# Kernel optimization log

Measured on AMD Instinct MI355X. Metric: run time of the kernel, lower is better.

The kernel has to match this reference:

```python
import jax, jax.numpy as jnp
import numpy as np

B, D, U = 64, 512, 512  # batch, input, units
EPS = 1e-5

def _ln(x, g, b, axes):
    m = jnp.mean(x, axis=axes, keepdims=True)
    v = jnp.mean((x - m) ** 2, axis=axes, keepdims=True)
    return (x - m) * jax.lax.rsqrt(v + EPS) * g + b

def setup_inputs() -> dict:
    key = jax.random.key(0)
    ks = jax.random.split(key, 8)
    w = lambda k, shape: 0.02 * jax.random.normal(k, shape, dtype=jnp.float32)
    return {
        "x": jax.random.normal(ks[0], (B, D), dtype=jnp.float32),
        "w1": w(ks[1], (1, D, U, 2)),
        "b1": jnp.zeros((1, D, U, 2), jnp.float32),
        "w21": w(ks[2], (1, D, U, 2)),
        "w22": w(ks[3], (1, D, U, 2)),
        "b21": jnp.zeros((1, D, U, 1), jnp.float32),
        "b22": jnp.zeros((1, D, U, 1), jnp.float32),
        "w3": w(ks[4], (1, D, U, 2)),
        "b3": jnp.zeros((1, D, U, 1), jnp.float32),
        "bias": jnp.zeros((U,), jnp.float32),
        "g0": jnp.ones((D,), jnp.float32), "be0": jnp.zeros((D,), jnp.float32),
        "g1": jnp.ones((D, U, 2), jnp.float32), "be1": jnp.zeros((D, U, 2), jnp.float32),
        "g2": jnp.ones((D, U, 2), jnp.float32), "be2": jnp.zeros((D, U, 2), jnp.float32),
        "g3": jnp.ones((D, U, 1), jnp.float32), "be3": jnp.zeros((D, U, 1), jnp.float32),
    }

def reference(x, w1, b1, w21, w22, b21, b22, w3, b3, bias,
              g0, be0, g1, be1, g2, be2, g3, be3):
    lrelu = lambda t: jnp.where(t >= 0, t, 0.01 * t)  # nn.LeakyReLU default slope
    xn = _ln(x, g0, be0, (-1,))[:, :, None, None]           # [B,D,1,1]
    l1 = lrelu(_ln(xn * w1 + b1, g1, be1, (1, 2, 3)))        # [B,D,U,2]
    l21 = jnp.sum(l1 * w21, axis=-1, keepdims=True) + b21    # [B,D,U,1]
    l22 = jnp.sum(l1 * w22, axis=-1, keepdims=True) + b22    # [B,D,U,1]
    l2 = lrelu(_ln(jnp.concatenate((l21, l22), axis=-1), g2, be2, (1, 2, 3)))  # [B,D,U,2]
    l3 = jnp.sum(l2 * w3, axis=-1, keepdims=True) + b3       # [B,D,U,1]
    out = _ln(l3, g3, be3, (1, 2, 3)) + xn                   # [B,D,U,1]
    out = lrelu(jnp.sum(out, axis=1) + bias[:, None])        # [B,U,1]
    return jnp.squeeze(out, axis=-1)                         # [B,U]
```

## Files before the change

kernel.cpp:

```cpp
#include <hip/hip_runtime.h>

#define EPS 1e-5f
constexpr float INV_N1 = 1.f / 524288.f;
constexpr float INV_N3 = 1.f / 262144.f;

__device__ __forceinline__ float lrelu(float y) { return fmaxf(y, 0.01f * y); }

template <int CTRL>
__device__ __forceinline__ float dppMov(float v) {
    return __int_as_float(__builtin_amdgcn_update_dpp(
        0, __float_as_int(v), CTRL, 0xF, 0xF, true));
}
__device__ __forceinline__ float rowSumDpp(float v) {
    v += dppMov<0x111>(v);
    v += dppMov<0x112>(v);
    v += dppMov<0x114>(v);
    v += dppMov<0x118>(v);
    return v;
}
__device__ __forceinline__ float quadSum(float v) {
    v += dppMov<0xB1>(v);
    v += dppMov<0x4E>(v);
    return v;
}
__device__ __forceinline__ float waveAllSum(float v) {
    v += __shfl_xor(v, 32); v += __shfl_xor(v, 16); v += __shfl_xor(v, 8);
    v += __shfl_xor(v, 4);  v += __shfl_xor(v, 2);  v += __shfl_xor(v, 1);
    return v;
}

__global__ void __launch_bounds__(256) kW(
    const float* __restrict__ w1, const float* __restrict__ b1,
    const float* __restrict__ g3, const float* __restrict__ be3,
    float* __restrict__ S1, float* __restrict__ S2, float* __restrict__ S11,
    float* __restrict__ S0b, float* __restrict__ Sb2,
    float* __restrict__ Gp, float* __restrict__ Bp) {
    int bid = blockIdx.x, tid = threadIdx.x;
    if (bid < 512) {
        const float4* wr = (const float4*)(w1 + bid * 1024);
        const float4* br = (const float4*)(b1 + bid * 1024);
        float4 w = wr[tid], b = br[tid];
        float s1  = w.x + w.y + w.z + w.w;
        float s2  = w.x * w.x + w.y * w.y + w.z * w.z + w.w * w.w;
        float s11 = w.x * b.x + w.y * b.y + w.z * b.z + w.w * b.w;
        float s0  = b.x + b.y + b.z + b.w;
        float sb2 = b.x * b.x + b.y * b.y + b.z * b.z + b.w * b.w;
        __shared__ float red[4][5];
        s1 = waveAllSum(s1); s2 = waveAllSum(s2); s11 = waveAllSum(s11);
        s0 = waveAllSum(s0); sb2 = waveAllSum(sb2);
        int wave = tid >> 6, lane = tid & 63;
        if (lane == 0) {
            red[wave][0] = s1; red[wave][1] = s2; red[wave][2] = s11;
            red[wave][3] = s0; red[wave][4] = sb2;
        }
        __syncthreads();
        if (tid == 0) {
            float a0 = 0, a1 = 0, a2 = 0, a3 = 0, a4 = 0;
            for (int w4 = 0; w4 < 4; ++w4) {
                a0 += red[w4][0]; a1 += red[w4][1]; a2 += red[w4][2];
                a3 += red[w4][3]; a4 += red[w4][4];
            }
            S1[bid] = a0; S2[bid] = a1; S11[bid] = a2;
            S0b[bid] = a3; Sb2[bid] = a4;
        }
    } else {
        int jj = bid - 512;
        float ag0 = 0, ag1 = 0, ab0 = 0, ab1 = 0;
#pragma unroll
        for (int r = 0; r < 8; ++r) {
            const float* gr = g3 + (jj * 8 + r) * 512;
            const float* br = be3 + (jj * 8 + r) * 512;
            ag0 += gr[tid];  ag1 += gr[tid + 256];
            ab0 += br[tid];  ab1 += br[tid + 256];
        }
        Gp[jj * 512 + tid] = ag0; Gp[jj * 512 + tid + 256] = ag1;
        Bp[jj * 512 + tid] = ab0; Bp[jj * 512 + tid + 256] = ab1;
    }
}

__global__ void __launch_bounds__(256) kB(
    const float* __restrict__ x, const float* __restrict__ g0,
    const float* __restrict__ be0,
    const float* __restrict__ S1, const float* __restrict__ S2,
    const float* __restrict__ S11, const float* __restrict__ S0b,
    const float* __restrict__ Sb2,
    const float* __restrict__ Gp, const float* __restrict__ Bp,
    float* __restrict__ xnp, float* __restrict__ rs1a, float* __restrict__ mm1a,
    float* __restrict__ Xs, float* __restrict__ G3s, float* __restrict__ Be3s) {
    int bid = blockIdx.x, tid = threadIdx.x;
    if (bid < 64) {
        int b = bid;
        float2 xv = ((const float2*)(x + b * 512))[tid];
        float sx = xv.x + xv.y;
        float sxx = xv.x * xv.x + xv.y * xv.y;
        __shared__ float red[4][3];
        __shared__ float bc[2];
        sx = waveAllSum(sx); sxx = waveAllSum(sxx);
        int wave = tid >> 6, lane = tid & 63;
        if (lane == 0) { red[wave][0] = sx; red[wave][1] = sxx; }
        __syncthreads();
        if (tid == 0) {
            float a = red[0][0] + red[1][0] + red[2][0] + red[3][0];
            float c = red[0][1] + red[1][1] + red[2][1] + red[3][1];
            float m = a * (1.f / 512.f);
            float var = c * (1.f / 512.f) - m * m;
            bc[0] = m; bc[1] = rsqrtf(var + EPS);
        }
        __syncthreads();
        float m = bc[0], rsd = bc[1];
        float2 g = ((const float2*)g0)[tid];
        float2 be = ((const float2*)be0)[tid];
        float xn0 = (xv.x - m) * rsd * g.x + be.x;
        float xn1 = (xv.y - m) * rsd * g.y + be.y;
        ((float2*)(xnp + b * 512))[tid] = make_float2(xn0, xn1);
        float2 s1 = ((const float2*)S1)[tid], s0b = ((const float2*)S0b)[tid];
        float2 s2 = ((const float2*)S2)[tid], s11 = ((const float2*)S11)[tid];
        float2 sb2 = ((const float2*)Sb2)[tid];
        float pm = fmaf(xn0, s1.x, s0b.x) + fmaf(xn1, s1.y, s0b.y);
        float pe = xn0 * xn0 * s2.x + 2.f * xn0 * s11.x + sb2.x
                 + xn1 * xn1 * s2.y + 2.f * xn1 * s11.y + sb2.y;
        float sxn = xn0 + xn1;
        pm = waveAllSum(pm); pe = waveAllSum(pe); sxn = waveAllSum(sxn);
        __syncthreads();
        if (lane == 0) { red[wave][0] = pm; red[wave][1] = pe; red[wave][2] = sxn; }
        __syncthreads();
        if (tid == 0) {
            float a = red[0][0] + red[1][0] + red[2][0] + red[3][0];
            float c = red[0][1] + red[1][1] + red[2][1] + red[3][1];
            float s = red[0][2] + red[1][2] + red[2][2] + red[3][2];
            float m1 = a * INV_N1;
            float e1 = c * INV_N1;
            float r = rsqrtf(e1 - m1 * m1 + EPS);
            rs1a[b] = r; mm1a[b] = m1 * r; Xs[b] = s;
        }
    } else if (bid == 64) {
        for (int u = tid; u < 512; u += 256) {
            float s = 0;
#pragma unroll 8
            for (int jj = 0; jj < 64; ++jj) s += Gp[jj * 512 + u];
            G3s[u] = s;
        }
    } else {
        for (int u = tid; u < 512; u += 256) {
            float s = 0;
#pragma unroll 8
            for (int jj = 0; jj < 64; ++jj) s += Bp[jj * 512 + u];
            Be3s[u] = s;
        }
    }
}

__global__ void __launch_bounds__(256) k1(
    const float* __restrict__ w1, const float* __restrict__ b1,
    const float* __restrict__ g1, const float* __restrict__ be1,
    const float* __restrict__ w21, const float* __restrict__ w22,
    const float* __restrict__ b21, const float* __restrict__ b22,
    const float* __restrict__ xnp, const float* __restrict__ rs1a,
    const float* __restrict__ mm1a, float* __restrict__ part1) {
    int bid = blockIdx.x, tid = threadIdx.x;
    int d = bid;
    __shared__ float xcol[64], scA[64], scB[64];
    __shared__ float2 red2[64][4][4];
    if (tid < 64) {
        xcol[tid] = xnp[tid * 512 + d];
        scA[tid] = rs1a[tid];
        scB[tid] = mm1a[tid];
    }
    int i0 = d * 512 + tid, i1 = i0 + 256;
    float2 W1a = ((const float2*)w1)[i0], B1a = ((const float2*)b1)[i0];
    float2 G1a = ((const float2*)g1)[i0], E1a = ((const float2*)be1)[i0];
    float2 Aa  = ((const float2*)w21)[i0], Ca = ((const float2*)w22)[i0];
    float Baa = b21[i0], Bca = b22[i0];
    float2 W1b = ((const float2*)w1)[i1], B1b = ((const float2*)b1)[i1];
    float2 G1b = ((const float2*)g1)[i1], E1b = ((const float2*)be1)[i1];
    float2 Ab  = ((const float2*)w21)[i1], Cb = ((const float2*)w22)[i1];
    float Bab = b21[i1], Bcb = b22[i1];
    __syncthreads();
    int wave = tid >> 6, lane = tid & 63;
    for (int b = 0; b < 64; ++b) {
        float xd = xcol[b], r1 = scA[b], mmv = scB[b];
        float t0 = fmaf(xd, W1a.x, B1a.x), t1 = fmaf(xd, W1a.y, B1a.y);
        float z0 = fmaf(t0, r1, -mmv), z1 = fmaf(t1, r1, -mmv);
        float y0 = fmaf(z0, G1a.x, E1a.x), y1 = fmaf(z1, G1a.y, E1a.y);
        float l0 = lrelu(y0), l1 = lrelu(y1);
        float c0 = fmaf(l0, Aa.x, fmaf(l1, Aa.y, Baa));
        float c1 = fmaf(l0, Ca.x, fmaf(l1, Ca.y, Bca));
        float v1 = c0 + c1;
        float v2 = fmaf(c0, c0, c1 * c1);
        t0 = fmaf(xd, W1b.x, B1b.x); t1 = fmaf(xd, W1b.y, B1b.y);
        z0 = fmaf(t0, r1, -mmv); z1 = fmaf(t1, r1, -mmv);
        y0 = fmaf(z0, G1b.x, E1b.x); y1 = fmaf(z1, G1b.y, E1b.y);
        l0 = lrelu(y0); l1 = lrelu(y1);
        c0 = fmaf(l0, Ab.x, fmaf(l1, Ab.y, Bab));
        c1 = fmaf(l0, Cb.x, fmaf(l1, Cb.y, Bcb));
        v1 += c0 + c1;
        v2 = fmaf(c0, c0, fmaf(c1, c1, v2));
        v1 = rowSumDpp(v1);
        v2 = rowSumDpp(v2);
        if ((lane & 15) == 15)
            red2[b][wave][lane >> 4] = make_float2(v1, v2);
    }
    __syncthreads();
    if (tid < 128) {
        int b = tid >> 1, k = tid & 1;
        float s = 0;
#pragma unroll
        for (int w = 0; w < 4; ++w)
#pragma unroll
            for (int r = 0; r < 4; ++r)
                s += ((const float*)&red2[b][w][r])[k];
        part1[bid * 128 + tid] = s;
    }
}

struct Wt { float2 W1, B1, G1, E1, A, C, G2, E2, W3; float Ba, Bc, B3, G3v; };

__global__ void __launch_bounds__(256) k2(
    const float* __restrict__ w1, const float* __restrict__ b1,
    const float* __restrict__ g1, const float* __restrict__ be1,
    const float* __restrict__ w21, const float* __restrict__ w22,
    const float* __restrict__ b21, const float* __restrict__ b22,
    const float* __restrict__ g2, const float* __restrict__ be2,
    const float* __restrict__ w3, const float* __restrict__ b3,
    const float* __restrict__ g3,
    const float* __restrict__ xnp, const float* __restrict__ rs1a,
    const float* __restrict__ mm1a, const float* __restrict__ part1,
    float* __restrict__ pp, float* __restrict__ qp) {
    int bu = blockIdx.x & 31, bd = blockIdx.x >> 5, tid = threadIdx.x;
    int lane = tid & 63, wave = tid >> 6;
    int ul = (lane >> 2) & 15, d0 = lane & 3;
    int u = bu * 16 + ul;
    int dl0 = wave * 8 + d0 * 2;
    __shared__ float4 sc[64];
    __shared__ float sxn[64][32];
    __shared__ float comb[4][64][16][3];
    __shared__ float tmp2[2][128];
    {
        int s = tid & 127, half = tid >> 7;
        float acc = 0;
        const float* p = part1 + half * 256 * 128 + s;
#pragma unroll 8
        for (int blk = 0; blk < 256; ++blk) acc += p[blk * 128];
        tmp2[half][s] = acc;
    }
    {
        float* cz = &comb[0][0][0][0];
        for (int t = tid; t < 4 * 64 * 16 * 3; t += 256) cz[t] = 0.f;
    }
    for (int idx = tid; idx < 2048; idx += 256)
        sxn[idx >> 5][idx & 31] = xnp[(idx >> 5) * 512 + bd * 32 + (idx & 31)];
    Wt wt[2];
#pragma unroll
    for (int j = 0; j < 2; ++j) {
        int d = bd * 32 + dl0 + j;
        int i = d * 512 + u;
        wt[j].W1 = ((const float2*)w1)[i];  wt[j].B1 = ((const float2*)b1)[i];
        wt[j].G1 = ((const float2*)g1)[i];  wt[j].E1 = ((const float2*)be1)[i];
        wt[j].A  = ((const float2*)w21)[i]; wt[j].C  = ((const float2*)w22)[i];
        wt[j].G2 = ((const float2*)g2)[i];  wt[j].E2 = ((const float2*)be2)[i];
        wt[j].W3 = ((const float2*)w3)[i];
        wt[j].Ba = b21[i]; wt[j].Bc = b22[i]; wt[j].B3 = b3[i]; wt[j].G3v = g3[i];
    }
    __syncthreads();
    if (tid < 64) {
        float ssum = tmp2[0][2 * tid] + tmp2[1][2 * tid];
        float s2sum = tmp2[0][2 * tid + 1] + tmp2[1][2 * tid + 1];
        float mm = ssum * INV_N1;
        float var = s2sum * INV_N1 - mm * mm;
        float r2 = rsqrtf(var + EPS);
        sc[tid] = make_float4(rs1a[tid], mm1a[tid], r2, mm * r2);
    }
    __syncthreads();
    for (int b = 0; b < 64; ++b) {
        float4 s4 = sc[b];
        float p = 0, q = 0, q2 = 0;
#pragma unroll
        for (int j = 0; j < 2; ++j) {
            float xd = sxn[b][dl0 + j];
            float t0 = fmaf(xd, wt[j].W1.x, wt[j].B1.x), t1 = fmaf(xd, wt[j].W1.y, wt[j].B1.y);
            float z0 = fmaf(t0, s4.x, -s4.y), z1 = fmaf(t1, s4.x, -s4.y);
            float y0 = fmaf(z0, wt[j].G1.x, wt[j].E1.x), y1 = fmaf(z1, wt[j].G1.y, wt[j].E1.y);
            float l0 = lrelu(y0), l1 = lrelu(y1);
            float c0 = fmaf(l0, wt[j].A.x, fmaf(l1, wt[j].A.y, wt[j].Ba));
            float c1 = fmaf(l0, wt[j].C.x, fmaf(l1, wt[j].C.y, wt[j].Bc));
            float z20 = fmaf(c0, s4.z, -s4.w), z21 = fmaf(c1, s4.z, -s4.w);
            float y20 = fmaf(z20, wt[j].G2.x, wt[j].E2.x), y21 = fmaf(z21, wt[j].G2.y, wt[j].E2.y);
            float m0 = lrelu(y20), m1v = lrelu(y21);
            float l3 = fmaf(m0, wt[j].W3.x, fmaf(m1v, wt[j].W3.y, wt[j].B3));
            p = fmaf(l3, wt[j].G3v, p); q += l3; q2 = fmaf(l3, l3, q2);
        }
        p = quadSum(p); q = quadSum(q); q2 = quadSum(q2);
        if (d0 < 3) {
            float v = (d0 == 0) ? p : ((d0 == 1) ? q : q2);
            comb[wave][b][ul][d0] += v;
        }
    }
    __syncthreads();
#pragma unroll
    for (int r = 0; r < 4; ++r) {
        int idx = r * 256 + tid;
        int b = idx >> 4, uu = idx & 15;
        float s = comb[0][b][uu][0] + comb[1][b][uu][0]
                + comb[2][b][uu][0] + comb[3][b][uu][0];
        pp[(bd * 64 + b) * 512 + bu * 16 + uu] = s;
    }
    if (tid < 128) {
        int b = tid >> 1, st = 1 + (tid & 1);
        float s = 0;
#pragma unroll
        for (int w = 0; w < 4; ++w)
#pragma unroll
            for (int uu = 0; uu < 16; ++uu) s += comb[w][b][uu][st];
        qp[(bd * 32 + bu) * 128 + b * 2 + (st - 1)] = s;
    }
}

__global__ void __launch_bounds__(512) k3(
    const float* __restrict__ pp, const float* __restrict__ qp,
    const float* __restrict__ G3s, const float* __restrict__ Be3s,
    const float* __restrict__ Xs, const float* __restrict__ bias,
    float* __restrict__ out) {
    int b = blockIdx.x, u = threadIdx.x;
    float q  = qp[u * 128 + b * 2 + 0];
    float q2 = qp[u * 128 + b * 2 + 1];
    __shared__ float red[8][2];
    __shared__ float bc2[2];
    float sq = waveAllSum(q), sq2 = waveAllSum(q2);
    int wave = u >> 6, lane = u & 63;
    if (lane == 0) { red[wave][0] = sq; red[wave][1] = sq2; }
    __syncthreads();
    if (u == 0) {
        float a = 0, c = 0;
        for (int w = 0; w < 8; ++w) { a += red[w][0]; c += red[w][1]; }
        float m3 = a * INV_N3;
        float e3 = c * INV_N3;
        bc2[0] = m3; bc2[1] = rsqrtf(e3 - m3 * m3 + EPS);
    }
    __syncthreads();
    float p = 0;
#pragma unroll 4
    for (int bd = 0; bd < 16; ++bd) p += pp[(bd * 64 + b) * 512 + u];
    float m3 = bc2[0], rs3 = bc2[1];
    float val = rs3 * (p - m3 * G3s[u]) + Be3s[u] + Xs[b] + bias[u];
    out[b * 512 + u] = lrelu(val);
}

extern "C" void kernel_launch(void* const* d_in, const int* in_sizes, int n_in,
                              void* d_out, int out_size, void* d_ws, size_t ws_size,
                              hipStream_t stream) {
    const float* x   = (const float*)d_in[0];
    const float* w1  = (const float*)d_in[1];
    const float* b1  = (const float*)d_in[2];
    const float* w21 = (const float*)d_in[3];
    const float* w22 = (const float*)d_in[4];
    const float* b21 = (const float*)d_in[5];
    const float* b22 = (const float*)d_in[6];
    const float* w3  = (const float*)d_in[7];
    const float* b3  = (const float*)d_in[8];
    const float* bias= (const float*)d_in[9];
    const float* g0  = (const float*)d_in[10];
    const float* be0 = (const float*)d_in[11];
    const float* g1  = (const float*)d_in[12];
    const float* be1 = (const float*)d_in[13];
    const float* g2  = (const float*)d_in[14];
    const float* be2 = (const float*)d_in[15];
    const float* g3  = (const float*)d_in[16];
    const float* be3 = (const float*)d_in[17];
    float* out = (float*)d_out;
    char* ws = (char*)d_ws;

    float* xn    = (float*)(ws);
    float* S1    = (float*)(ws + 131072);
    float* S2    = (float*)(ws + 133120);
    float* S11   = (float*)(ws + 135168);
    float* S0b   = (float*)(ws + 137216);
    float* Sb2   = (float*)(ws + 139264);
    float* rs1a  = (float*)(ws + 141312);
    float* mm1a  = (float*)(ws + 141568);
    float* Xs    = (float*)(ws + 141824);
    float* G3s   = (float*)(ws + 142080);
    float* Be3s  = (float*)(ws + 144128);
    float* Gp    = (float*)(ws + 146176);
    float* Bp    = (float*)(ws + 277248);
    float* part1 = (float*)(ws + 408320);
    float* qp    = (float*)(ws + 670464);
    float* pp    = (float*)(ws + 932608);

    hipLaunchKernelGGL(kW, dim3(576), dim3(256), 0, stream,
                       w1, b1, g3, be3, S1, S2, S11, S0b, Sb2, Gp, Bp);
    hipLaunchKernelGGL(kB, dim3(66), dim3(256), 0, stream,
                       x, g0, be0, S1, S2, S11, S0b, Sb2, Gp, Bp,
                       xn, rs1a, mm1a, Xs, G3s, Be3s);
    hipLaunchKernelGGL(k1, dim3(512), dim3(256), 0, stream,
                       w1, b1, g1, be1, w21, w22, b21, b22, xn, rs1a, mm1a, part1);
    hipLaunchKernelGGL(k2, dim3(512), dim3(256), 0, stream,
                       w1, b1, g1, be1, w21, w22, b21, b22, g2, be2, w3, b3, g3,
                       xn, rs1a, mm1a, part1, pp, qp);
    hipLaunchKernelGGL(k3, dim3(64), dim3(512), 0, stream,
                       pp, qp, G3s, Be3s, Xs, bias, out);
}
```

Baseline: 72.10 us.

## Eliminate the stats kernel by fusing its work into neighbouring kernels

Result: slower. 90.37 us (+25.3%).

```diff
diff --git a/kernel.cpp b/kernel.cpp
--- a/kernel.cpp
+++ b/kernel.cpp
@@ -29,13 +29,19 @@
     return v;
 }
 
-__global__ void __launch_bounds__(256) kW(
+__global__ void __launch_bounds__(256) kA(
     const float* __restrict__ w1, const float* __restrict__ b1,
     const float* __restrict__ g3, const float* __restrict__ be3,
+    const float* __restrict__ x, const float* __restrict__ g0,
+    const float* __restrict__ be0,
     float* __restrict__ S1, float* __restrict__ S2, float* __restrict__ S11,
     float* __restrict__ S0b, float* __restrict__ Sb2,
-    float* __restrict__ Gp, float* __restrict__ Bp) {
+    float* __restrict__ Gp, float* __restrict__ Bp,
+    float* __restrict__ xnp, float* __restrict__ Xs) {
     int bid = blockIdx.x, tid = threadIdx.x;
+    int wave = tid >> 6, lane = tid & 63;
+    __shared__ float red[4][5];
+    __shared__ float bc[2];
     if (bid < 512) {
         const float4* wr = (const float4*)(w1 + bid * 1024);
         const float4* br = (const float4*)(b1 + bid * 1024);
@@ -45,10 +51,8 @@
         float s11 = w.x * b.x + w.y * b.y + w.z * b.z + w.w * b.w;
         float s0  = b.x + b.y + b.z + b.w;
         float sb2 = b.x * b.x + b.y * b.y + b.z * b.z + b.w * b.w;
-        __shared__ float red[4][5];
         s1 = waveAllSum(s1); s2 = waveAllSum(s2); s11 = waveAllSum(s11);
         s0 = waveAllSum(s0); sb2 = waveAllSum(sb2);
-        int wave = tid >> 6, lane = tid & 63;
         if (lane == 0) {
             red[wave][0] = s1; red[wave][1] = s2; red[wave][2] = s11;
             red[wave][3] = s0; red[wave][4] = sb2;
@@ -63,7 +67,7 @@
             S1[bid] = a0; S2[bid] = a1; S11[bid] = a2;
             S0b[bid] = a3; Sb2[bid] = a4;
         }
-    } else {
+    } else if (bid < 576) {
         int jj = bid - 512;
         float ag0 = 0, ag1 = 0, ab0 = 0, ab1 = 0;
 #pragma unroll
@@ -75,78 +79,31 @@
         }
         Gp[jj * 512 + tid] = ag0; Gp[jj * 512 + tid + 256] = ag1;
         Bp[jj * 512 + tid] = ab0; Bp[jj * 512 + tid + 256] = ab1;
-    }
-}
-
-__global__ void __launch_bounds__(256) kB(
-    const float* __restrict__ x, const float* __restrict__ g0,
-    const float* __restrict__ be0,
-    const float* __restrict__ S1, const float* __restrict__ S2,
-    const float* __restrict__ S11, const float* __restrict__ S0b,
-    const float* __restrict__ Sb2,
-    const float* __restrict__ Gp, const float* __restrict__ Bp,
-    float* __restrict__ xnp, float* __restrict__ rs1a, float* __restrict__ mm1a,
-    float* __restrict__ Xs, float* __restrict__ G3s, float* __restrict__ Be3s) {
-    int bid = blockIdx.x, tid = threadIdx.x;
-    if (bid < 64) {
-        int b = bid;
+    } else {
+        int b = bid - 576;
         float2 xv = ((const float2*)(x + b * 512))[tid];
-        float sx = xv.x + xv.y;
-        float sxx = xv.x * xv.x + xv.y * xv.y;
-        __shared__ float red[4][3];
-        __shared__ float bc[2];
+        float sx = xv.x + xv.y, sxx = xv.x * xv.x + xv.y * xv.y;
         sx = waveAllSum(sx); sxx = waveAllSum(sxx);
-        int wave = tid >> 6, lane = tid & 63;
         if (lane == 0) { red[wave][0] = sx; red[wave][1] = sxx; }
         __syncthreads();
         if (tid == 0) {
-            float a = red[0][0] + red[1][0] + red[2][0] + red[3][0];
+            float s = red[0][0] + red[1][0] + red[2][0] + red[3][0];
             float c = red[0][1] + red[1][1] + red[2][1] + red[3][1];
-            float m = a * (1.f / 512.f);
+            float m = s * (1.f / 512.f);
             float var = c * (1.f / 512.f) - m * m;
             bc[0] = m; bc[1] = rsqrtf(var + EPS);
         }
         __syncthreads();
         float m = bc[0], rsd = bc[1];
-        float2 g = ((const float2*)g0)[tid];
-        float2 be = ((const float2*)be0)[tid];
+        float2 g = ((const float2*)g0)[tid], be = ((const float2*)be0)[tid];
         float xn0 = (xv.x - m) * rsd * g.x + be.x;
         float xn1 = (xv.y - m) * rsd * g.y + be.y;
         ((float2*)(xnp + b * 512))[tid] = make_float2(xn0, xn1);
-        float2 s1 = ((const float2*)S1)[tid], s0b = ((const float2*)S0b)[tid];
-        float2 s2 = ((const float2*)S2)[tid], s11 = ((const float2*)S11)[tid];
-        float2 sb2 = ((const float2*)Sb2)[tid];
-        float pm = fmaf(xn0, s1.x, s0b.x) + fmaf(xn1, s1.y, s0b.y);
-        float pe = xn0 * xn0 * s2.x + 2.f * xn0 * s11.x + sb2.x
-                 + xn1 * xn1 * s2.y + 2.f * xn1 * s11.y + sb2.y;
-        float sxn = xn0 + xn1;
-        pm = waveAllSum(pm); pe = waveAllSum(pe); sxn = waveAllSum(sxn);
-        __syncthreads();
-        if (lane == 0) { red[wave][0] = pm; red[wave][1] = pe; red[wave][2] = sxn; }
-        __syncthreads();
-        if (tid == 0) {
-            float a = red[0][0] + red[1][0] + red[2][0] + red[3][0];
-            float c = red[0][1] + red[1][1] + red[2][1] + red[3][1];
-            float s = red[0][2] + red[1][2] + red[2][2] + red[3][2];
-            float m1 = a * INV_N1;
-            float e1 = c * INV_N1;
-            float r = rsqrtf(e1 - m1 * m1 + EPS);
-            rs1a[b] = r; mm1a[b] = m1 * r; Xs[b] = s;
-        }
-    } else if (bid == 64) {
-        for (int u = tid; u < 512; u += 256) {
-            float s = 0;
-#pragma unroll 8
-            for (int jj = 0; jj < 64; ++jj) s += Gp[jj * 512 + u];
-            G3s[u] = s;
-        }
-    } else {
-        for (int u = tid; u < 512; u += 256) {
-            float s = 0;
-#pragma unroll 8
-            for (int jj = 0; jj < 64; ++jj) s += Bp[jj * 512 + u];
-            Be3s[u] = s;
-        }
+        float sxn = waveAllSum(xn0 + xn1);
+        __syncthreads();
+        if (lane == 0) red[wave][0] = sxn;
+        __syncthreads();
+        if (tid == 0) Xs[b] = red[0][0] + red[1][0] + red[2][0] + red[3][0];
     }
 }
 
@@ -155,16 +112,63 @@
     const float* __restrict__ g1, const float* __restrict__ be1,
     const float* __restrict__ w21, const float* __restrict__ w22,
     const float* __restrict__ b21, const float* __restrict__ b22,
-    const float* __restrict__ xnp, const float* __restrict__ rs1a,
-    const float* __restrict__ mm1a, float* __restrict__ part1) {
+    const float* __restrict__ xnp,
+    const float* __restrict__ S1, const float* __restrict__ S2,
+    const float* __restrict__ S11, const float* __restrict__ S0b,
+    const float* __restrict__ Sb2,
+    float* __restrict__ rs1a, float* __restrict__ mm1a,
+    float* __restrict__ part1) {
     int bid = blockIdx.x, tid = threadIdx.x;
     int d = bid;
+    int wave = tid >> 6, lane = tid & 63;
     __shared__ float xcol[64], scA[64], scB[64];
     __shared__ float2 red2[64][4][4];
-    if (tid < 64) {
-        xcol[tid] = xnp[tid * 512 + d];
-        scA[tid] = rs1a[tid];
-        scB[tid] = mm1a[tid];
+    __shared__ float stat2[64][2];
+    __shared__ float redc[4][2];
+    __shared__ float cbc[2];
+    {
+        float s1a = S1[tid],  s1b = S1[tid + 256];
+        float s2a = S2[tid],  s2b = S2[tid + 256];
+        float sca = S11[tid], scb = S11[tid + 256];
+        float cs0 = S0b[tid] + S0b[tid + 256];
+        float csb = Sb2[tid] + Sb2[tid + 256];
+        cs0 = waveAllSum(cs0); csb = waveAllSum(csb);
+        if (lane == 0) { redc[wave][0] = cs0; redc[wave][1] = csb; }
+        for (int b = 0; b < 64; ++b) {
+            float xn0 = xnp[b * 512 + tid], xn1 = xnp[b * 512 + tid + 256];
+            float pm = fmaf(xn0, s1a, xn1 * s1b);
+            float pe = xn0 * xn0 * s2a + 2.f * xn0 * sca
+                     + xn1 * xn1 * s2b + 2.f * xn1 * scb;
+            pm = rowSumDpp(pm);
+            pe = rowSumDpp(pe);
+            if ((lane & 15) == 15)
+                red2[b][wave][lane >> 4] = make_float2(pm, pe);
+        }
+        __syncthreads();
+        if (tid == 0)
+            cbc[0] = redc[0][0] + redc[1][0] + redc[2][0] + redc[3][0];
+        else if (tid == 1)
+            cbc[1] = redc[0][1] + redc[1][1] + redc[2][1] + redc[3][1];
+        if (tid < 128) {
+            int b = tid >> 1, k = tid & 1;
+            float s = 0;
+#pragma unroll
+            for (int w = 0; w < 4; ++w)
+#pragma unroll
+                for (int r = 0; r < 4; ++r)
+                    s += ((const float*)&red2[b][w][r])[k];
+            stat2[b][k] = s;
+        }
+        __syncthreads();
+        if (tid < 64) {
+            float pm = stat2[tid][0] + cbc[0];
+            float pe = stat2[tid][1] + cbc[1];
+            float m1 = pm * INV_N1, e1 = pe * INV_N1;
+            float r = rsqrtf(e1 - m1 * m1 + EPS);
+            scA[tid] = r; scB[tid] = m1 * r;
+            xcol[tid] = xnp[tid * 512 + d];
+            if (bid == 0) { rs1a[tid] = r; mm1a[tid] = m1 * r; }
+        }
     }
     int i0 = d * 512 + tid, i1 = i0 + 256;
     float2 W1a = ((const float2*)w1)[i0], B1a = ((const float2*)b1)[i0];
@@ -176,7 +180,6 @@
     float2 Ab  = ((const float2*)w21)[i1], Cb = ((const float2*)w22)[i1];
     float Bab = b21[i1], Bcb = b22[i1];
     __syncthreads();
-    int wave = tid >> 6, lane = tid & 63;
     for (int b = 0; b < 64; ++b) {
         float xd = xcol[b], r1 = scA[b], mmv = scB[b];
         float t0 = fmaf(xd, W1a.x, B1a.x), t1 = fmaf(xd, W1a.y, B1a.y);
@@ -317,10 +320,16 @@
 
 __global__ void __launch_bounds__(512) k3(
     const float* __restrict__ pp, const float* __restrict__ qp,
-    const float* __restrict__ G3s, const float* __restrict__ Be3s,
+    const float* __restrict__ Gp, const float* __restrict__ Bp,
     const float* __restrict__ Xs, const float* __restrict__ bias,
     float* __restrict__ out) {
     int b = blockIdx.x, u = threadIdx.x;
+    float g3s = 0, be3s = 0;
+#pragma unroll 8
+    for (int jj = 0; jj < 64; ++jj) {
+        g3s  += Gp[jj * 512 + u];
+        be3s += Bp[jj * 512 + u];
+    }
     float q  = qp[u * 128 + b * 2 + 0];
     float q2 = qp[u * 128 + b * 2 + 1];
     __shared__ float red[8][2];
@@ -341,7 +350,7 @@
 #pragma unroll 4
     for (int bd = 0; bd < 16; ++bd) p += pp[(bd * 64 + b) * 512 + u];
     float m3 = bc2[0], rs3 = bc2[1];
-    float val = rs3 * (p - m3 * G3s[u]) + Be3s[u] + Xs[b] + bias[u];
+    float val = rs3 * (p - m3 * g3s) + be3s + Xs[b] + bias[u];
     out[b * 512 + u] = lrelu(val);
 }
 
@@ -378,24 +387,21 @@
     float* rs1a  = (float*)(ws + 141312);
     float* mm1a  = (float*)(ws + 141568);
     float* Xs    = (float*)(ws + 141824);
-    float* G3s   = (float*)(ws + 142080);
-    float* Be3s  = (float*)(ws + 144128);
     float* Gp    = (float*)(ws + 146176);
     float* Bp    = (float*)(ws + 277248);
     float* part1 = (float*)(ws + 408320);
     float* qp    = (float*)(ws + 670464);
     float* pp    = (float*)(ws + 932608);
 
-    hipLaunchKernelGGL(kW, dim3(576), dim3(256), 0, stream,
-                       w1, b1, g3, be3, S1, S2, S11, S0b, Sb2, Gp, Bp);
-    hipLaunchKernelGGL(kB, dim3(66), dim3(256), 0, stream,
-                       x, g0, be0, S1, S2, S11, S0b, Sb2, Gp, Bp,
-                       xn, rs1a, mm1a, Xs, G3s, Be3s);
+    hipLaunchKernelGGL(kA, dim3(640), dim3(256), 0, stream,
+                       w1, b1, g3, be3, x, g0, be0,
+                       S1, S2, S11, S0b, Sb2, Gp, Bp, xn, Xs);
     hipLaunchKernelGGL(k1, dim3(512), dim3(256), 0, stream,
-                       w1, b1, g1, be1, w21, w22, b21, b22, xn, rs1a, mm1a, part1);
+                       w1, b1, g1, be1, w21, w22, b21, b22, xn,
+                       S1, S2, S11, S0b, Sb2, rs1a, mm1a, part1);
     hipLaunchKernelGGL(k2, dim3(512), dim3(256), 0, stream,
                        w1, b1, g1, be1, w21, w22, b21, b22, g2, be2, w3, b3, g3,
                        xn, rs1a, mm1a, part1, pp, qp);
     hipLaunchKernelGGL(k3, dim3(64), dim3(512), 0, stream,
-                       pp, qp, G3s, Be3s, Xs, bias, out);
-}
+                       pp, qp, Gp, Bp, Xs, bias, out);
+}
```
